# Performance work log

Measured on AMD Instinct MI355X. Metric: run time of the kernel, lower is better.

The kernel has to match this reference:

```python
import jax, jax.numpy as jnp
import numpy as np

EPS = 1e-12  # torch F.normalize default eps

def setup_inputs() -> dict:
    key = jax.random.key(0)
    k1, k2, k3 = jax.random.split(key, 3)
    B, C, H, W = 32, 512, 64, 64
    HEADS = 8
    local_feature = jax.random.normal(k1, (B, C, H, W), dtype=jnp.float32)
    global_feature = jax.random.normal(k2, (B, C, H, W), dtype=jnp.float32)
    temperature = jnp.ones((HEADS, 1, 1), dtype=jnp.float32)
    proj_w = jax.random.normal(k3, (C, C), dtype=jnp.float32) * 0.02  # project_out 1x1 conv weight [out,in]
    return {"local_feature": local_feature, "global_feature": global_feature,
            "temperature": temperature, "proj_w": proj_w}

def _l2norm(x):
    # F.normalize(x, dim=-1): x / max(||x||_2, eps)
    n = jnp.sqrt(jnp.sum(x * x, axis=-1, keepdims=True))
    return x / jnp.maximum(n, EPS)

def reference(local_feature, global_feature, temperature, proj_w):
    B, C, H, W = local_feature.shape
    heads = temperature.shape[0]
    d = C // heads
    split = lambda x: x.reshape(B, heads, d, H * W)  # b (head c) h w -> b head c (hw)
    q = _l2norm(split(local_feature))
    k = _l2norm(split(global_feature))
    v = split(global_feature)
    # channel-attention: [b,h,d,d] score matrix (d small), softmax over last dim
    attn = jax.nn.softmax(jnp.einsum('bhcn,bhdn->bhcd', q, k) * temperature, axis=-1)
    out = jnp.einsum('bhcd,bhdn->bhcn', attn, v).reshape(B, C, H, W)
    # project_out: 1x1 conv, no bias -> channel GEMM
    return jnp.einsum('oc,bchw->bohw', proj_w, out)
```

## Files before the change

### kernel.cpp

```cpp
#include <hip/hip_runtime.h>
#include <stdint.h>

#define B_N 32
#define C_N 512
#define HEADS_N 8
#define D_N 64
#define N_SP 4096

typedef __attribute__((ext_vector_type(8))) short short8;
typedef __attribute__((ext_vector_type(4))) float f32x4;

__device__ __forceinline__ unsigned int f2bf1(float x) {
  unsigned int u = __float_as_uint(x);
  return (u + 0x7fffu + ((u >> 16) & 1u)) >> 16;
}
__device__ __forceinline__ unsigned int packbf(float lo, float hi) {
  return f2bf1(lo) | (f2bf1(hi) << 16);
}

__global__ __launch_bounds__(256, 6) void attn_partial_kernel(
    const float* __restrict__ localf, const float* __restrict__ globf,
    float* __restrict__ pS, float* __restrict__ pssq, int splitk)
{
  const int h = blockIdx.x, b = blockIdx.y, chunk = blockIdx.z;
  const int t = threadIdx.x;
  const int lane = t & 63, w = t >> 6;
  const int rquad = t >> 4;
  const int c4 = t & 15;

  __shared__ unsigned short tA[64 * 72];
  __shared__ unsigned short tB[64 * 72];

  const float* Qb = localf + ((size_t)(b * C_N + h * D_N)) * N_SP;
  const float* Kb = globf  + ((size_t)(b * C_N + h * D_N)) * N_SP;

  const int iters = 64 / splitk;
  const int it0 = chunk * iters;

  f32x4 acc[2][2];
#pragma unroll
  for (int i = 0; i < 2; ++i)
#pragma unroll
    for (int j = 0; j < 2; ++j) acc[i][j] = (f32x4){0.f, 0.f, 0.f, 0.f};

  float ssqA[4] = {0.f, 0.f, 0.f, 0.f}, ssqB[4] = {0.f, 0.f, 0.f, 0.f};
  f32x4 qa[4], ka[4];

  {
    int n0 = it0 * 64 + c4 * 4;
#pragma unroll
    for (int i = 0; i < 4; ++i) {
      int row = i * 16 + rquad;
      qa[i] = *(const f32x4*)(Qb + (size_t)row * N_SP + n0);
      ka[i] = *(const f32x4*)(Kb + (size_t)row * N_SP + n0);
    }
  }

  const int lr = lane & 15, lq = lane >> 4;
  const int rbase = (w >> 1) * 32, cbase = (w & 1) * 32;

  for (int it = it0; it < it0 + iters; ++it) {
#pragma unroll
    for (int i = 0; i < 4; ++i) {
      int row = i * 16 + rquad;
      f32x4 q = qa[i], k = ka[i];
      ssqA[i] += q[0]*q[0] + q[1]*q[1] + q[2]*q[2] + q[3]*q[3];
      ssqB[i] += k[0]*k[0] + k[1]*k[1] + k[2]*k[2] + k[3]*k[3];
      uint2 qp; qp.x = packbf(q[0], q[1]); qp.y = packbf(q[2], q[3]);
      uint2 kp; kp.x = packbf(k[0], k[1]); kp.y = packbf(k[2], k[3]);
      *(uint2*)(tA + row * 72 + c4 * 4) = qp;
      *(uint2*)(tB + row * 72 + c4 * 4) = kp;
    }
    __syncthreads();
    if (it + 1 < it0 + iters) {
      int n0 = (it + 1) * 64 + c4 * 4;
#pragma unroll
      for (int i = 0; i < 4; ++i) {
        int row = i * 16 + rquad;
        qa[i] = *(const f32x4*)(Qb + (size_t)row * N_SP + n0);
        ka[i] = *(const f32x4*)(Kb + (size_t)row * N_SP + n0);
      }
    }
#pragma unroll
    for (int s = 0; s < 2; ++s) {
      short8 af[2], bf[2];
#pragma unroll
      for (int mt = 0; mt < 2; ++mt)
        af[mt] = *(const short8*)(tA + (rbase + mt * 16 + lr) * 72 + (s * 4 + lq) * 8);
#pragma unroll
      for (int nt = 0; nt < 2; ++nt)
        bf[nt] = *(const short8*)(tB + (cbase + nt * 16 + lr) * 72 + (s * 4 + lq) * 8);
#pragma unroll
      for (int mt = 0; mt < 2; ++mt)
#pragma unroll
        for (int nt = 0; nt < 2; ++nt)
          acc[mt][nt] = __builtin_amdgcn_mfma_f32_16x16x32_bf16(
              af[mt], bf[nt], acc[mt][nt], 0, 0, 0);
    }
    __syncthreads();
  }

  const size_t obase = (size_t)(b * HEADS_N + h) * (size_t)splitk + chunk;

#pragma unroll
  for (int i = 0; i < 4; ++i) {
    float a = ssqA[i], bb = ssqB[i];
#pragma unroll
    for (int m = 8; m >= 1; m >>= 1) {
      a  += __shfl_xor(a, m, 64);
      bb += __shfl_xor(bb, m, 64);
    }
    if (c4 == 0) {
      int row = i * 16 + rquad;
      pssq[obase * 128 + row]      = a;
      pssq[obase * 128 + 64 + row] = bb;
    }
  }

  float* ps = pS + obase * 4096;
#pragma unroll
  for (int mt = 0; mt < 2; ++mt)
#pragma unroll
    for (int nt = 0; nt < 2; ++nt)
#pragma unroll
      for (int r = 0; r < 4; ++r) {
        int rg = rbase + mt * 16 + lq * 4 + r;
        int cg = cbase + nt * 16 + lr;
        ps[rg * 64 + cg] = acc[mt][nt][r];
      }
}

__global__ __launch_bounds__(256) void attn_combine_kernel(
    const float* __restrict__ pS, const float* __restrict__ pssq,
    const float* __restrict__ temp, float* __restrict__ attn_out, int splitk)
{
  const int h = blockIdx.x, b = blockIdx.y, t = threadIdx.x;
  __shared__ float S[64 * 68];
  __shared__ float invv[128];

  const size_t base = (size_t)(b * HEADS_N + h) * (size_t)splitk;

  float r[16];
#pragma unroll
  for (int i = 0; i < 16; ++i) r[i] = 0.f;
  for (int c = 0; c < splitk; ++c) {
    const float* p = pS + (base + c) * 4096;
#pragma unroll
    for (int i = 0; i < 16; ++i) r[i] += p[t + 256 * i];
  }
  if (t < 128) {
    float s = 0.f;
    for (int c = 0; c < splitk; ++c) s += pssq[(base + c) * 128 + t];
    invv[t] = 1.0f / fmaxf(sqrtf(s), 1e-12f);
  }
#pragma unroll
  for (int i = 0; i < 16; ++i) {
    int e = t + 256 * i;
    S[(e >> 6) * 68 + (e & 63)] = r[i];
  }
  __syncthreads();

  const float tval = temp[h];
#pragma unroll
  for (int i = 0; i < 16; ++i) {
    int e = t + 256 * i;
    int rw = e >> 6, cl = e & 63;
    S[rw * 68 + cl] *= invv[rw] * invv[64 + cl] * tval;
  }
  __syncthreads();

  if (t < 64) {
    float mx = -1e30f;
#pragma unroll 8
    for (int j = 0; j < 64; ++j) mx = fmaxf(mx, S[t * 68 + j]);
    float sum = 0.f;
#pragma unroll 8
    for (int j = 0; j < 64; ++j) {
      float e = __expf(S[t * 68 + j] - mx);
      S[t * 68 + j] = e;
      sum += e;
    }
    float inv = 1.0f / sum;
    float* op = attn_out + ((size_t)((b * HEADS_N + h) * 64 + t)) * 64;
#pragma unroll 8
    for (int j = 0; j < 64; ++j) op[j] = S[t * 68 + j] * inv;
  }
}

__global__ __launch_bounds__(256) void fold_kernel(
    const float* __restrict__ proj, const float* __restrict__ attn,
    unsigned short* __restrict__ Mout)
{
  const int h = blockIdx.x, b = blockIdx.y, zh = blockIdx.z;
  const int t = threadIdx.x;
  __shared__ float A_[64 * 64];
  const float* ap = attn + (size_t)(b * HEADS_N + h) * 4096;
#pragma unroll
  for (int i = 0; i < 16; ++i) A_[i * 256 + t] = ap[i * 256 + t];
  __syncthreads();
  const int e = t & 63, w = t >> 6;
  float col[64];
#pragma unroll
  for (int cc = 0; cc < 64; ++cc) col[cc] = A_[cc * 64 + e];
  unsigned short* mb = Mout + (size_t)b * C_N * C_N + (size_t)h * 64 + e;
  for (int i = 0; i < 16; ++i) {
    int o = zh * 64 + i * 4 + w;
    const float* pr = proj + (size_t)o * C_N + h * 64;
    float s = 0.f;
#pragma unroll
    for (int cc = 0; cc < 64; cc += 4) {
      f32x4 p = *(const f32x4*)(pr + cc);
      s += p[0]*col[cc] + p[1]*col[cc+1] + p[2]*col[cc+2] + p[3]*col[cc+3];
    }
    mb[(size_t)o * C_N] = (unsigned short)f2bf1(s);
  }
}

__global__ __launch_bounds__(256, 4) void final_gemm_kernel(
    const unsigned short* __restrict__ Mw, const float* __restrict__ globf,
    float* __restrict__ outp)
{
  const int nt0 = blockIdx.x;
  const int mt0 = blockIdx.y;
  const int b   = blockIdx.z;
  const int t = threadIdx.x, lane = t & 63, w = t >> 6;
  const int lr = lane & 15, lq = lane >> 4;

  __shared__ unsigned short tA[128 * 72];
  __shared__ unsigned short tB[128 * 72];

  const unsigned short* Mb = Mw + ((size_t)b * C_N + mt0 * 128) * C_N;
  const float* Gb = globf + (size_t)b * C_N * N_SP + nt0 * 128;

  f32x4 acc[4][4];
#pragma unroll
  for (int i = 0; i < 4; ++i)
#pragma unroll
    for (int j = 0; j < 4; ++j) acc[i][j] = (f32x4){0.f, 0.f, 0.f, 0.f};

  const int mq = (w >> 1) * 64, nq2 = (w & 1) * 64;
  const int nq = t & 31, kg = t >> 5;

  int4 av[4];
  f32x4 gv[8];

  {
#pragma unroll
    for (int i = 0; i < 4; ++i) {
      int u = t + 256 * i; int o = u >> 3, j = u & 7;
      av[i] = *(const int4*)(Mb + (size_t)o * C_N + j * 8);
    }
    const float* gp = Gb + (size_t)(kg * 8) * N_SP + nq * 4;
#pragma unroll
    for (int i = 0; i < 8; ++i) gv[i] = *(const f32x4*)(gp + (size_t)i * N_SP);
  }

  for (int kb = 0; kb < 8; ++kb) {
#pragma unroll
    for (int i = 0; i < 4; ++i) {
      int u = t + 256 * i; int o = u >> 3, j = u & 7;
      *(int4*)(tA + o * 72 + j * 8) = av[i];
    }
#pragma unroll
    for (int r = 0; r < 4; ++r) {
      int n = nq * 4 + r;
      int4 pk;
      pk.x = (int)packbf(gv[0][r], gv[1][r]);
      pk.y = (int)packbf(gv[2][r], gv[3][r]);
      pk.z = (int)packbf(gv[4][r], gv[5][r]);
      pk.w = (int)packbf(gv[6][r], gv[7][r]);
      int gph = kg ^ (nq & 7);
      *(int4*)(tB + n * 72 + gph * 8) = pk;
    }
    __syncthreads();
    if (kb < 7) {
      int kn = (kb + 1) * 64;
#pragma unroll
      for (int i = 0; i < 4; ++i) {
        int u = t + 256 * i; int o = u >> 3, j = u & 7;
        av[i] = *(const int4*)(Mb + (size_t)o * C_N + kn + j * 8);
      }
      const float* gp = Gb + (size_t)(kn + kg * 8) * N_SP + nq * 4;
#pragma unroll
      for (int i = 0; i < 8; ++i) gv[i] = *(const f32x4*)(gp + (size_t)i * N_SP);
    }
#pragma unroll
    for (int s = 0; s < 2; ++s) {
      short8 af[4], bf[4];
#pragma unroll
      for (int mt = 0; mt < 4; ++mt)
        af[mt] = *(const short8*)(tA + (mq + mt * 16 + lr) * 72 + (s * 4 + lq) * 8);
#pragma unroll
      for (int nt = 0; nt < 4; ++nt) {
        int n = nq2 + nt * 16 + lr;
        int g2 = (s * 4 + lq) ^ ((n >> 2) & 7);
        bf[nt] = *(const short8*)(tB + n * 72 + g2 * 8);
      }
#pragma unroll
      for (int mt = 0; mt < 4; ++mt)
#pragma unroll
        for (int nt = 0; nt < 4; ++nt)
          acc[mt][nt] = __builtin_amdgcn_mfma_f32_16x16x32_bf16(
              af[mt], bf[nt], acc[mt][nt], 0, 0, 0);
    }
    __syncthreads();
  }

  float* E = (float*)tA;
  float* E_w = E + w * (16 * 68);
#pragma unroll
  for (int mt = 0; mt < 4; ++mt) {
    __syncthreads();
#pragma unroll
    for (int nt = 0; nt < 4; ++nt)
#pragma unroll
      for (int r = 0; r < 4; ++r)
        E_w[(lq * 4 + r) * 68 + nt * 16 + lr] = acc[mt][nt][r];
    __syncthreads();
    float* ob = outp + ((size_t)(b * C_N + mt0 * 128 + mq + mt * 16)) * N_SP
              + nt0 * 128 + nq2;
#pragma unroll
    for (int rr = 0; rr < 4; ++rr) {
      int row = rr * 4 + lq;
      f32x4 v = *(const f32x4*)(E_w + row * 68 + lr * 4);
      *(f32x4*)(ob + (size_t)row * N_SP + lr * 4) = v;
    }
  }
}

extern "C" void kernel_launch(void* const* d_in, const int* in_sizes, int n_in,
                              void* d_out, int out_size, void* d_ws, size_t ws_size,
                              hipStream_t stream) {
  const float* localf = (const float*)d_in[0];
  const float* globf  = (const float*)d_in[1];
  const float* temp   = (const float*)d_in[2];
  const float* proj   = (const float*)d_in[3];
  float* out = (float*)d_out;

  const size_t ATTN_BYTES = (size_t)B_N * HEADS_N * 64 * 64 * sizeof(float);
  const size_t M_BYTES    = (size_t)B_N * C_N * C_N * sizeof(unsigned short);

  int splitk = 8;
  while (splitk > 1) {
    size_t need = ATTN_BYTES + M_BYTES +
                  (size_t)B_N * HEADS_N * (size_t)splitk * (4096 + 128) * sizeof(float);
    if (need <= ws_size) break;
    splitk >>= 1;
  }

  float* attn_ws = (float*)d_ws;
  unsigned short* M_ws = (unsigned short*)((char*)d_ws + ATTN_BYTES);
  float* pS   = (float*)((char*)d_ws + ATTN_BYTES + M_BYTES);
  float* pssq = pS + (size_t)B_N * HEADS_N * (size_t)splitk * 4096;

  attn_partial_kernel<<<dim3(HEADS_N, B_N, splitk), 256, 0, stream>>>(
      localf, globf, pS, pssq, splitk);
  attn_combine_kernel<<<dim3(HEADS_N, B_N), 256, 0, stream>>>(
      pS, pssq, temp, attn_ws, splitk);
  fold_kernel<<<dim3(HEADS_N, B_N, 8), 256, 0, stream>>>(proj, attn_ws, M_ws);
  final_gemm_kernel<<<dim3(32, 4, B_N), 256, 0, stream>>>(M_ws, globf, out);
}
```

Measured before the change: 1.047 ms.

## Fuse softmax combine with projection fold; add nontemporal loads and stores

Merges the attention combine and fold kernels into one kernel, so the softmaxed attention stays in shared memory and is multiplied by proj chunks staged through LDS. This removes the attn workspace round trip and one launch, but the fold now runs on only 256 blocks instead of 2048, which cuts parallelism. The Q/K loads in the partial kernel and the partial-sum and final output stores become nontemporal. The final GEMM drops its LDS-staged epilogue for direct scattered scalar stores, and launch bounds change in two kernels.

```diff
diff --git a/kernel.cpp b/kernel.cpp
--- a/kernel.cpp
+++ b/kernel.cpp
@@ -18,7 +18,7 @@
   return f2bf1(lo) | (f2bf1(hi) << 16);
 }
 
-__global__ __launch_bounds__(256, 6) void attn_partial_kernel(
+__global__ __launch_bounds__(256) void attn_partial_kernel(
     const float* __restrict__ localf, const float* __restrict__ globf,
     float* __restrict__ pS, float* __restrict__ pssq, int splitk)
 {
@@ -51,8 +51,8 @@
 #pragma unroll
     for (int i = 0; i < 4; ++i) {
       int row = i * 16 + rquad;
-      qa[i] = *(const f32x4*)(Qb + (size_t)row * N_SP + n0);
-      ka[i] = *(const f32x4*)(Kb + (size_t)row * N_SP + n0);
+      qa[i] = __builtin_nontemporal_load((const f32x4*)(Qb + (size_t)row * N_SP + n0));
+      ka[i] = __builtin_nontemporal_load((const f32x4*)(Kb + (size_t)row * N_SP + n0));
     }
   }
 
@@ -77,8 +77,8 @@
 #pragma unroll
       for (int i = 0; i < 4; ++i) {
         int row = i * 16 + rquad;
-        qa[i] = *(const f32x4*)(Qb + (size_t)row * N_SP + n0);
-        ka[i] = *(const f32x4*)(Kb + (size_t)row * N_SP + n0);
+        qa[i] = __builtin_nontemporal_load((const f32x4*)(Qb + (size_t)row * N_SP + n0));
+        ka[i] = __builtin_nontemporal_load((const f32x4*)(Kb + (size_t)row * N_SP + n0));
       }
     }
 #pragma unroll
@@ -126,17 +126,20 @@
       for (int r = 0; r < 4; ++r) {
         int rg = rbase + mt * 16 + lq * 4 + r;
         int cg = cbase + nt * 16 + lr;
-        ps[rg * 64 + cg] = acc[mt][nt][r];
-      }
-}
-
-__global__ __launch_bounds__(256) void attn_combine_kernel(
+        __builtin_nontemporal_store(acc[mt][nt][r], ps + rg * 64 + cg);
+      }
+}
+
+__global__ __launch_bounds__(256) void combine_fold_kernel(
     const float* __restrict__ pS, const float* __restrict__ pssq,
-    const float* __restrict__ temp, float* __restrict__ attn_out, int splitk)
+    const float* __restrict__ temp, const float* __restrict__ proj,
+    unsigned short* __restrict__ Mout, int splitk)
 {
   const int h = blockIdx.x, b = blockIdx.y, t = threadIdx.x;
-  __shared__ float S[64 * 68];
+  __shared__ float ST[64 * 69];
+  __shared__ float SP[128 * 68];
   __shared__ float invv[128];
+  float* S = SP;
 
   const size_t base = (size_t)(b * HEADS_N + h) * (size_t)splitk;
 
@@ -174,49 +177,48 @@
 #pragma unroll 8
     for (int j = 0; j < 64; ++j) mx = fmaxf(mx, S[t * 68 + j]);
     float sum = 0.f;
+    float ex[64];
 #pragma unroll 8
     for (int j = 0; j < 64; ++j) {
       float e = __expf(S[t * 68 + j] - mx);
-      S[t * 68 + j] = e;
+      ex[j] = e;
       sum += e;
     }
     float inv = 1.0f / sum;
-    float* op = attn_out + ((size_t)((b * HEADS_N + h) * 64 + t)) * 64;
 #pragma unroll 8
-    for (int j = 0; j < 64; ++j) op[j] = S[t * 68 + j] * inv;
-  }
-}
-
-__global__ __launch_bounds__(256) void fold_kernel(
-    const float* __restrict__ proj, const float* __restrict__ attn,
-    unsigned short* __restrict__ Mout)
-{
-  const int h = blockIdx.x, b = blockIdx.y, zh = blockIdx.z;
-  const int t = threadIdx.x;
-  __shared__ float A_[64 * 64];
-  const float* ap = attn + (size_t)(b * HEADS_N + h) * 4096;
-#pragma unroll
-  for (int i = 0; i < 16; ++i) A_[i * 256 + t] = ap[i * 256 + t];
+    for (int j = 0; j < 64; ++j) ST[j * 69 + t] = ex[j] * inv;
+  }
   __syncthreads();
+
   const int e = t & 63, w = t >> 6;
-  float col[64];
-#pragma unroll
-  for (int cc = 0; cc < 64; ++cc) col[cc] = A_[cc * 64 + e];
   unsigned short* mb = Mout + (size_t)b * C_N * C_N + (size_t)h * 64 + e;
-  for (int i = 0; i < 16; ++i) {
-    int o = zh * 64 + i * 4 + w;
-    const float* pr = proj + (size_t)o * C_N + h * 64;
-    float s = 0.f;
-#pragma unroll
-    for (int cc = 0; cc < 64; cc += 4) {
-      f32x4 p = *(const f32x4*)(pr + cc);
-      s += p[0]*col[cc] + p[1]*col[cc+1] + p[2]*col[cc+2] + p[3]*col[cc+3];
-    }
-    mb[(size_t)o * C_N] = (unsigned short)f2bf1(s);
-  }
-}
-
-__global__ __launch_bounds__(256, 4) void final_gemm_kernel(
+  const float* STrow = ST + (size_t)e * 69;
+
+  for (int chunk = 0; chunk < 4; ++chunk) {
+#pragma unroll
+    for (int i = 0; i < 32; ++i) {
+      int row = i * 4 + w;
+      SP[row * 68 + e] = proj[(size_t)(chunk * 128 + row) * C_N + h * 64 + e];
+    }
+    __syncthreads();
+#pragma unroll 4
+    for (int oi = 0; oi < 32; ++oi) {
+      int ol = oi * 4 + w;
+      const float* Pr = SP + ol * 68;
+      float s = 0.f;
+#pragma unroll
+      for (int cc = 0; cc < 64; cc += 4) {
+        s += Pr[cc]     * STrow[cc]     + Pr[cc + 1] * STrow[cc + 1]
+           + Pr[cc + 2] * STrow[cc + 2] + Pr[cc + 3] * STrow[cc + 3];
+      }
+      int o = chunk * 128 + ol;
+      mb[(size_t)o * C_N] = (unsigned short)f2bf1(s);
+    }
+    __syncthreads();
+  }
+}
+
+__global__ __launch_bounds__(256, 2) void final_gemm_kernel(
     const unsigned short* __restrict__ Mw, const float* __restrict__ globf,
     float* __restrict__ outp)
 {
@@ -306,26 +308,16 @@
     __syncthreads();
   }
 
-  float* E = (float*)tA;
-  float* E_w = E + w * (16 * 68);
-#pragma unroll
-  for (int mt = 0; mt < 4; ++mt) {
-    __syncthreads();
+  float* ob = outp + ((size_t)(b * C_N + mt0 * 128 + mq)) * N_SP + nt0 * 128 + nq2;
+#pragma unroll
+  for (int mt = 0; mt < 4; ++mt)
 #pragma unroll
     for (int nt = 0; nt < 4; ++nt)
 #pragma unroll
       for (int r = 0; r < 4; ++r)
-        E_w[(lq * 4 + r) * 68 + nt * 16 + lr] = acc[mt][nt][r];
-    __syncthreads();
-    float* ob = outp + ((size_t)(b * C_N + mt0 * 128 + mq + mt * 16)) * N_SP
-              + nt0 * 128 + nq2;
-#pragma unroll
-    for (int rr = 0; rr < 4; ++rr) {
-      int row = rr * 4 + lq;
-      f32x4 v = *(const f32x4*)(E_w + row * 68 + lr * 4);
-      *(f32x4*)(ob + (size_t)row * N_SP + lr * 4) = v;
-    }
-  }
+        __builtin_nontemporal_store(
+            acc[mt][nt][r],
+            ob + (size_t)(mt * 16 + lq * 4 + r) * N_SP + nt * 16 + lr);
 }
 
 extern "C" void kernel_launch(void* const* d_in, const int* in_sizes, int n_in,
@@ -337,26 +329,23 @@
   const float* proj   = (const float*)d_in[3];
   float* out = (float*)d_out;
 
-  const size_t ATTN_BYTES = (size_t)B_N * HEADS_N * 64 * 64 * sizeof(float);
-  const size_t M_BYTES    = (size_t)B_N * C_N * C_N * sizeof(unsigned short);
+  const size_t M_BYTES = (size_t)B_N * C_N * C_N * sizeof(unsigned short);
 
   int splitk = 8;
   while (splitk > 1) {
-    size_t need = ATTN_BYTES + M_BYTES +
+    size_t need = M_BYTES +
                   (size_t)B_N * HEADS_N * (size_t)splitk * (4096 + 128) * sizeof(float);
     if (need <= ws_size) break;
     splitk >>= 1;
   }
 
-  float* attn_ws = (float*)d_ws;
-  unsigned short* M_ws = (unsigned short*)((char*)d_ws + ATTN_BYTES);
-  float* pS   = (float*)((char*)d_ws + ATTN_BYTES + M_BYTES);
+  unsigned short* M_ws = (unsigned short*)d_ws;
+  float* pS   = (float*)((char*)d_ws + M_BYTES);
   float* pssq = pS + (size_t)B_N * HEADS_N * (size_t)splitk * 4096;
 
   attn_partial_kernel<<<dim3(HEADS_N, B_N, splitk), 256, 0, stream>>>(
       localf, globf, pS, pssq, splitk);
-  attn_combine_kernel<<<dim3(HEADS_N, B_N), 256, 0, stream>>>(
-      pS, pssq, temp, attn_ws, splitk);
-  fold_kernel<<<dim3(HEADS_N, B_N, 8), 256, 0, stream>>>(proj, attn_ws, M_ws);
+  combine_fold_kernel<<<dim3(HEADS_N, B_N), 256, 0, stream>>>(
+      pS, pssq, temp, proj, M_ws, splitk);
   final_gemm_kernel<<<dim3(32, 4, B_N), 256, 0, stream>>>(M_ws, globf, out);
 }
```

Result: faster. 925.6 us (-11.6%).
